# Kernel optimization log

Measured on AMD Instinct MI355X. Metric: run time of the kernel, lower is better.

Reference implementation:

```python
import jax, jax.numpy as jnp
import numpy as np

IN_CH = 64
INTER = IN_CH // 2
B, H, W = 2, 80, 80


def setup_inputs() -> dict:
    key = jax.random.key(0)
    k = jax.random.split(key, 5)
    s = 1.0 / np.sqrt(IN_CH)
    return {
        "x": jax.random.normal(k[0], (B, IN_CH, H, W), dtype=jnp.float32),
        "g_w": jax.random.normal(k[1], (INTER, IN_CH), dtype=jnp.float32) * s,
        "theta_w": jax.random.normal(k[2], (INTER, IN_CH), dtype=jnp.float32) * s,
        "phi_w": jax.random.normal(k[3], (INTER, IN_CH), dtype=jnp.float32) * s,
        "w_w": jax.random.normal(k[4], (IN_CH, INTER), dtype=jnp.float32) * (1.0 / np.sqrt(INTER)),
    }


def reference(x, g_w, theta_w, phi_w, w_w):
    # Non-local block: 1x1 convs (bias=False) are channel matmuls over N=H*W positions.
    Bc, C, Hh, Ww = x.shape
    N = Hh * Ww
    xf = x.reshape(Bc, C, N)                            # [B, C, N]
    g = jnp.einsum('ic,bcn->bni', g_w, xf)              # [B, N, inter]
    theta = jnp.einsum('ic,bcn->bni', theta_w, xf)      # [B, N, inter]
    phi = jnp.einsum('ic,bcn->bin', phi_w, xf)          # [B, inter, N]
    affinity = jax.nn.softmax(jnp.einsum('bni,bim->bnm', theta, phi), axis=-1)  # [B, N, N]
    y = jnp.einsum('bnm,bmi->bni', affinity, g)         # [B, N, inter]
    y = jnp.einsum('ci,bni->bcn', w_w, y).reshape(Bc, C, Hh, Ww)
    return x + y
```

## Files before the change

### kernel.cpp

```cpp
#include <hip/hip_runtime.h>
#include <math.h>

#define BATCH 2
#define CH    64
#define INTER 32
#define NPOS  6400
#define LOG2E 1.44269504088896f
#define SPLIT 10
#define TPB   5

typedef _Float16 f16x8 __attribute__((ext_vector_type(8)));
typedef _Float16 f16x2 __attribute__((ext_vector_type(2)));
typedef _Float16 h4    __attribute__((ext_vector_type(4)));
typedef float    f32x4 __attribute__((ext_vector_type(4)));

static __device__ __forceinline__ f16x2 pkrtz(float a, float b) {
    return __builtin_bit_cast(f16x2, __builtin_amdgcn_cvt_pkrtz(a, b));
}

__global__ __launch_bounds__(256) void nlb_proj_kernel(
    const float* __restrict__ x,
    const float* __restrict__ g_w,
    const float* __restrict__ th_w,
    const float* __restrict__ ph_w,
    _Float16* __restrict__ Qh, _Float16* __restrict__ Kh,
    _Float16* __restrict__ Vt)
{
    const int b  = blockIdx.z;
    const int p  = blockIdx.y;
    const int n0 = blockIdx.x * 64;
    const int t  = threadIdx.x;
    const int w  = __builtin_amdgcn_readfirstlane(t) >> 6;
    const int lane = t & 63;

    const float* wsrc = (p == 0) ? th_w : (p == 1) ? ph_w : g_w;
    const float* xg = x + (size_t)b * CH * NPOS + n0 + lane;

    float xr[64];
    #pragma unroll
    for (int c = 0; c < 64; c++) xr[c] = xg[(size_t)c * NPOS];

    __shared__ float buf[32][65];

    float accs[8];
    #pragma unroll
    for (int rr = 0; rr < 8; rr++) {
        const int row = w * 8 + rr;
        const float* wr = wsrc + row * 64;
        float a0 = 0.f, a1 = 0.f, a2 = 0.f, a3 = 0.f;
        #pragma unroll
        for (int c = 0; c < 16; c++) {
            a0 += wr[c]      * xr[c];
            a1 += wr[c + 16] * xr[c + 16];
            a2 += wr[c + 32] * xr[c + 32];
            a3 += wr[c + 48] * xr[c + 48];
        }
        accs[rr] = (a0 + a1) + (a2 + a3);
    }

    if (p == 2) {
        const int n   = n0 + lane;
        const int kk  = n & 127;
        const int g   = kk >> 4, qd = (kk >> 2) & 3, rr2 = kk & 3;
        const int slot = (g >> 1) * 32 + qd * 8 + (g & 1) * 4 + rr2;
        const size_t col = (size_t)(n >> 7) * 128 + slot;
        #pragma unroll
        for (int rr = 0; rr < 8; rr++)
            Vt[((size_t)b * 32 + w * 8 + rr) * NPOS + col] = (_Float16)accs[rr];
        return;
    }

    #pragma unroll
    for (int rr = 0; rr < 8; rr++) buf[w * 8 + rr][lane] = accs[rr];
    __syncthreads();

    const float scale = (p == 0) ? LOG2E : 1.f;
    _Float16* dst = (p == 0) ? Qh : Kh;
    const int pos = t >> 2, ic = t & 3;
    f16x8 hv;
    #pragma unroll
    for (int j = 0; j < 8; j++)
        hv[j] = (_Float16)(buf[ic * 8 + j][pos] * scale);
    *(f16x8*)(dst + ((size_t)b * NPOS + n0 + pos) * 32 + ic * 8) = hv;
}

__global__ __launch_bounds__(256) void nlb_flash_kernel(
    const _Float16* __restrict__ Qh, const _Float16* __restrict__ Kh,
    const _Float16* __restrict__ Vt,
    _Float16* __restrict__ Opart, float2* __restrict__ ml)
{
    __shared__ __align__(16) _Float16 ks[2][128][40];
    __shared__ __align__(16) _Float16 vs[2][32][136];

    const int b     = blockIdx.z;
    const int split = blockIdx.y;
    const int t     = threadIdx.x;
    const int w     = t >> 6;
    const int lane  = t & 63;
    const int n16   = lane & 15;
    const int quad  = lane >> 4;
    const int q0    = blockIdx.x * 64 + w * 16;

    const f16x8 qa = *(const f16x8*)(Qh + ((size_t)b * NPOS + q0 + n16) * 32 + quad * 8);

    const _Float16* KB = Kh + (size_t)b * NPOS * 32;
    const _Float16* VB = Vt + (size_t)b * 32 * NPOS;

    f32x4 o0 = (f32x4)0.f;
    f32x4 o1 = (f32x4)0.f;
    float runm = -1e30f, lsum = 0.f;

    const int key0 = t >> 2, part = t & 3, key1 = key0 + 64;
    const int dim0 = t >> 4, kp   = t & 15, dim1 = dim0 + 16;

    const int kt0 = split * TPB;
    f16x8 kr0, kr1, vr0, vr1;
    {
        const int k0 = kt0 * 128;
        kr0 = *(const f16x8*)(KB + (size_t)(k0 + key0) * 32 + part * 8);
        kr1 = *(const f16x8*)(KB + (size_t)(k0 + key1) * 32 + part * 8);
        vr0 = *(const f16x8*)(VB + (size_t)dim0 * NPOS + k0 + kp * 8);
        vr1 = *(const f16x8*)(VB + (size_t)dim1 * NPOS + k0 + kp * 8);
    }

    for (int i = 0; i < TPB; i++) {
        const int cur = i & 1;
        *(f16x8*)&ks[cur][key0][part * 8] = kr0;
        *(f16x8*)&ks[cur][key1][part * 8] = kr1;
        *(f16x8*)&vs[cur][dim0][kp * 8]   = vr0;
        *(f16x8*)&vs[cur][dim1][kp * 8]   = vr1;
        __syncthreads();

        if (i + 1 < TPB) {
            const int k0n = (kt0 + i + 1) * 128;
            kr0 = *(const f16x8*)(KB + (size_t)(k0n + key0) * 32 + part * 8);
            kr1 = *(const f16x8*)(KB + (size_t)(k0n + key1) * 32 + part * 8);
            vr0 = *(const f16x8*)(VB + (size_t)dim0 * NPOS + k0n + kp * 8);
            vr1 = *(const f16x8*)(VB + (size_t)dim1 * NPOS + k0n + kp * 8);
        }

        f32x4 sc[8];
        #pragma unroll
        for (int g = 0; g < 8; g++) {
            f16x8 kf = *(const f16x8*)&ks[cur][g * 16 + n16][quad * 8];
            f32x4 z = (f32x4)0.f;
            sc[g] = __builtin_amdgcn_mfma_f32_16x16x32_f16(kf, qa, z, 0, 0, 0);
        }

        float m = fmaxf(fmaxf(sc[0][0], sc[0][1]), fmaxf(sc[0][2], sc[0][3]));
        #pragma unroll
        for (int g = 1; g < 8; g++) {
            float mg = fmaxf(fmaxf(sc[g][0], sc[g][1]), fmaxf(sc[g][2], sc[g][3]));
            m = fmaxf(m, mg);
        }
        m = fmaxf(m, __shfl_xor(m, 16));
        m = fmaxf(m, __shfl_xor(m, 32));
        float nm = fmaxf(runm, m);
        float a  = __builtin_amdgcn_exp2f(runm - nm);
        runm = nm;
        float ls = 0.f;
        #pragma unroll
        for (int g = 0; g < 8; g++) {
            #pragma unroll
            for (int r = 0; r < 4; r++) {
                float p = __builtin_amdgcn_exp2f(sc[g][r] - nm);
                sc[g][r] = p;
                ls += p;
            }
        }
        lsum = lsum * a + ls;
        o0 *= a;
        o1 *= a;

        #pragma unroll
        for (int kc = 0; kc < 4; kc++) {
            union { f16x8 v; f16x2 h2[4]; } pb;
            pb.h2[0] = pkrtz(sc[kc * 2][0],     sc[kc * 2][1]);
            pb.h2[1] = pkrtz(sc[kc * 2][2],     sc[kc * 2][3]);
            pb.h2[2] = pkrtz(sc[kc * 2 + 1][0], sc[kc * 2 + 1][1]);
            pb.h2[3] = pkrtz(sc[kc * 2 + 1][2], sc[kc * 2 + 1][3]);
            f16x8 v0 = *(const f16x8*)&vs[cur][n16][kc * 32 + quad * 8];
            f16x8 v1 = *(const f16x8*)&vs[cur][16 + n16][kc * 32 + quad * 8];
            o0 = __builtin_amdgcn_mfma_f32_16x16x32_f16(v0, pb.v, o0, 0, 0, 0);
            o1 = __builtin_amdgcn_mfma_f32_16x16x32_f16(v1, pb.v, o1, 0, 0, 0);
        }
    }

    lsum += __shfl_xor(lsum, 16);
    lsum += __shfl_xor(lsum, 32);
    float invl = 1.f / lsum;
    const size_t base = ((size_t)(b * SPLIT + split) * NPOS + q0 + n16) * 32;
    h4 h0, h1;
    #pragma unroll
    for (int r = 0; r < 4; r++) {
        h0[r] = (_Float16)(o0[r] * invl);
        h1[r] = (_Float16)(o1[r] * invl);
    }
    *(h4*)(Opart + base + quad * 4)      = h0;
    *(h4*)(Opart + base + 16 + quad * 4) = h1;
    if (quad == 0)
        ml[(size_t)(b * SPLIT + split) * NPOS + q0 + n16] = make_float2(runm, lsum);
}

__global__ __launch_bounds__(256) void nlb_combine_kernel(
    const _Float16* __restrict__ Opart, const float2* __restrict__ ml,
    const float* __restrict__ w_w, const float* __restrict__ x,
    float* __restrict__ out)
{
    __shared__ float wf[64][33];
    __shared__ float wts[32][12];
    __shared__ float of[32][33];

    const int b  = blockIdx.y;
    const int q0 = blockIdx.x * 32;
    const int t  = threadIdx.x;

    for (int idx = t; idx < 2048; idx += 256) wf[idx >> 5][idx & 31] = w_w[idx];

    if (t < 32) {
        float2 v[SPLIT];
        float m = -1e30f;
        #pragma unroll
        for (int s = 0; s < SPLIT; s++) {
            v[s] = ml[(size_t)(b * SPLIT + s) * NPOS + q0 + t];
            m = fmaxf(m, v[s].x);
        }
        float suml = 0.f;
        #pragma unroll
        for (int s = 0; s < SPLIT; s++) {
            float wgt = __builtin_amdgcn_exp2f(v[s].x - m) * v[s].y;
            wts[t][s] = wgt;
            suml += wgt;
        }
        float inv = 1.f / suml;
        #pragma unroll
        for (int s = 0; s < SPLIT; s++) wts[t][s] *= inv;
    }
    __syncthreads();

    {
        const int q = t >> 3, dg = t & 7;
        float a0 = 0.f, a1 = 0.f, a2 = 0.f, a3 = 0.f;
        #pragma unroll
        for (int s = 0; s < SPLIT; s++) {
            h4 hv = *(const h4*)(Opart +
                ((size_t)(b * SPLIT + s) * NPOS + q0 + q) * 32 + dg * 4);
            float c = wts[q][s];
            a0 += c * (float)hv[0]; a1 += c * (float)hv[1];
            a2 += c * (float)hv[2]; a3 += c * (float)hv[3];
        }
        of[q][dg * 4]     = a0; of[q][dg * 4 + 1] = a1;
        of[q][dg * 4 + 2] = a2; of[q][dg * 4 + 3] = a3;
    }
    __syncthreads();

    {
        const int q = t & 31, cg = t >> 5;
        const float* xb = x   + (size_t)b * CH * NPOS + q0 + q;
        float*       ob = out + (size_t)b * CH * NPOS + q0 + q;
        #pragma unroll
        for (int cc = 0; cc < 8; cc++) {
            int ch = cg * 8 + cc;
            float acc = 0.f;
            #pragma unroll
            for (int i = 0; i < 32; i++) acc += wf[ch][i] * of[q][i];
            ob[(size_t)ch * NPOS] = acc + xb[(size_t)ch * NPOS];
        }
    }
}

extern "C" void kernel_launch(void* const* d_in, const int* in_sizes, int n_in,
                              void* d_out, int out_size, void* d_ws, size_t ws_size,
                              hipStream_t stream) {
    const float* x    = (const float*)d_in[0];
    const float* g_w  = (const float*)d_in[1];
    const float* th_w = (const float*)d_in[2];
    const float* ph_w = (const float*)d_in[3];
    const float* w_w  = (const float*)d_in[4];
    float* out = (float*)d_out;

    const size_t SZ = (size_t)BATCH * NPOS * INTER;
    _Float16* Qh = (_Float16*)d_ws;
    _Float16* Kh = Qh + SZ;
    _Float16* Vt = Kh + SZ;
    _Float16* Opart = Vt + SZ;
    float2*   ml    = (float2*)(Opart + SZ * SPLIT);

    nlb_proj_kernel<<<dim3(NPOS / 64, 3, BATCH), 256, 0, stream>>>(
        x, g_w, th_w, ph_w, Qh, Kh, Vt);
    nlb_flash_kernel<<<dim3(NPOS / 64, SPLIT, BATCH), 256, 0, stream>>>(
        Qh, Kh, Vt, Opart, ml);
    nlb_combine_kernel<<<dim3(NPOS / 32, BATCH), 256, 0, stream>>>(
        Opart, ml, w_w, x, out);
}
```

Measured before the change: 107.5 us.

## Fuse split-combine and output projection into flash kernel via last-block atomic counter

Removes the separate combine kernel. Each flash block bumps a per-query-block atomic counter after a threadfence, and the last of the SPLIT blocks to finish merges the partial outputs, applies the w_w projection and adds the residual. The counters are zeroed in the projection kernel. This saves one kernel launch and its gap, at the cost of an extra fence, atomics, a serialized tail on one block per query tile, and a union shared-memory layout.

```diff
diff --git a/kernel.cpp b/kernel.cpp
--- a/kernel.cpp
+++ b/kernel.cpp
@@ -8,6 +8,7 @@
 #define LOG2E 1.44269504088896f
 #define SPLIT 10
 #define TPB   5
+#define NQB   (NPOS / 64)
 
 typedef _Float16 f16x8 __attribute__((ext_vector_type(8)));
 typedef _Float16 f16x2 __attribute__((ext_vector_type(2)));
@@ -24,7 +25,7 @@
     const float* __restrict__ th_w,
     const float* __restrict__ ph_w,
     _Float16* __restrict__ Qh, _Float16* __restrict__ Kh,
-    _Float16* __restrict__ Vt)
+    _Float16* __restrict__ Vt, int* __restrict__ cnt)
 {
     const int b  = blockIdx.z;
     const int p  = blockIdx.y;
@@ -33,6 +34,8 @@
     const int w  = __builtin_amdgcn_readfirstlane(t) >> 6;
     const int lane = t & 63;
 
+    if (p == 0 && t == 0) cnt[b * NQB + blockIdx.x] = 0;
+
     const float* wsrc = (p == 0) ? th_w : (p == 1) ? ph_w : g_w;
     const float* xg = x + (size_t)b * CH * NPOS + n0 + lane;
 
@@ -84,13 +87,29 @@
     *(f16x8*)(dst + ((size_t)b * NPOS + n0 + pos) * 32 + ic * 8) = hv;
 }
 
+struct SmemFlash {
+    _Float16 ks[2][128][40];
+    _Float16 vs[2][32][136];
+};
+struct SmemTail {
+    float wf[64][33];
+    float wts[64][12];
+    float of[64][33];
+};
+
 __global__ __launch_bounds__(256) void nlb_flash_kernel(
     const _Float16* __restrict__ Qh, const _Float16* __restrict__ Kh,
     const _Float16* __restrict__ Vt,
-    _Float16* __restrict__ Opart, float2* __restrict__ ml)
+    _Float16* __restrict__ Opart, float2* __restrict__ ml,
+    int* __restrict__ cnt,
+    const float* __restrict__ w_w, const float* __restrict__ x,
+    float* __restrict__ out)
 {
-    __shared__ __align__(16) _Float16 ks[2][128][40];
-    __shared__ __align__(16) _Float16 vs[2][32][136];
+    constexpr size_t SMEM_BYTES =
+        sizeof(SmemFlash) > sizeof(SmemTail) ? sizeof(SmemFlash) : sizeof(SmemTail);
+    __shared__ __align__(16) char smem[SMEM_BYTES];
+    __shared__ int lastFlag;
+    SmemFlash* sf = (SmemFlash*)smem;
 
     const int b     = blockIdx.z;
     const int split = blockIdx.y;
@@ -125,10 +144,10 @@
 
     for (int i = 0; i < TPB; i++) {
         const int cur = i & 1;
-        *(f16x8*)&ks[cur][key0][part * 8] = kr0;
-        *(f16x8*)&ks[cur][key1][part * 8] = kr1;
-        *(f16x8*)&vs[cur][dim0][kp * 8]   = vr0;
-        *(f16x8*)&vs[cur][dim1][kp * 8]   = vr1;
+        *(f16x8*)&sf->ks[cur][key0][part * 8] = kr0;
+        *(f16x8*)&sf->ks[cur][key1][part * 8] = kr1;
+        *(f16x8*)&sf->vs[cur][dim0][kp * 8]   = vr0;
+        *(f16x8*)&sf->vs[cur][dim1][kp * 8]   = vr1;
         __syncthreads();
 
         if (i + 1 < TPB) {
@@ -142,7 +161,7 @@
         f32x4 sc[8];
         #pragma unroll
         for (int g = 0; g < 8; g++) {
-            f16x8 kf = *(const f16x8*)&ks[cur][g * 16 + n16][quad * 8];
+            f16x8 kf = *(const f16x8*)&sf->ks[cur][g * 16 + n16][quad * 8];
             f32x4 z = (f32x4)0.f;
             sc[g] = __builtin_amdgcn_mfma_f32_16x16x32_f16(kf, qa, z, 0, 0, 0);
         }
@@ -179,8 +198,8 @@
             pb.h2[1] = pkrtz(sc[kc * 2][2],     sc[kc * 2][3]);
             pb.h2[2] = pkrtz(sc[kc * 2 + 1][0], sc[kc * 2 + 1][1]);
             pb.h2[3] = pkrtz(sc[kc * 2 + 1][2], sc[kc * 2 + 1][3]);
-            f16x8 v0 = *(const f16x8*)&vs[cur][n16][kc * 32 + quad * 8];
-            f16x8 v1 = *(const f16x8*)&vs[cur][16 + n16][kc * 32 + quad * 8];
+            f16x8 v0 = *(const f16x8*)&sf->vs[cur][n16][kc * 32 + quad * 8];
+            f16x8 v1 = *(const f16x8*)&sf->vs[cur][16 + n16][kc * 32 + quad * 8];
             o0 = __builtin_amdgcn_mfma_f32_16x16x32_f16(v0, pb.v, o0, 0, 0, 0);
             o1 = __builtin_amdgcn_mfma_f32_16x16x32_f16(v1, pb.v, o1, 0, 0, 0);
         }
@@ -200,70 +219,72 @@
     *(h4*)(Opart + base + 16 + quad * 4) = h1;
     if (quad == 0)
         ml[(size_t)(b * SPLIT + split) * NPOS + q0 + n16] = make_float2(runm, lsum);
-}
-
-__global__ __launch_bounds__(256) void nlb_combine_kernel(
-    const _Float16* __restrict__ Opart, const float2* __restrict__ ml,
-    const float* __restrict__ w_w, const float* __restrict__ x,
-    float* __restrict__ out)
-{
-    __shared__ float wf[64][33];
-    __shared__ float wts[32][12];
-    __shared__ float of[32][33];
-
-    const int b  = blockIdx.y;
-    const int q0 = blockIdx.x * 32;
-    const int t  = threadIdx.x;
-
-    for (int idx = t; idx < 2048; idx += 256) wf[idx >> 5][idx & 31] = w_w[idx];
-
-    if (t < 32) {
+
+    __threadfence();
+    __syncthreads();
+    if (t == 0) {
+        int old = atomicAdd(&cnt[b * NQB + blockIdx.x], 1);
+        lastFlag = (old == SPLIT - 1);
+    }
+    __syncthreads();
+    if (!lastFlag) return;
+    __threadfence();
+
+    SmemTail* st = (SmemTail*)smem;
+    const int q0b = blockIdx.x * 64;
+
+    for (int idx = t; idx < 2048; idx += 256)
+        st->wf[idx >> 5][idx & 31] = w_w[idx];
+
+    if (t < 64) {
         float2 v[SPLIT];
         float m = -1e30f;
         #pragma unroll
         for (int s = 0; s < SPLIT; s++) {
-            v[s] = ml[(size_t)(b * SPLIT + s) * NPOS + q0 + t];
+            v[s] = ml[(size_t)(b * SPLIT + s) * NPOS + q0b + t];
             m = fmaxf(m, v[s].x);
         }
         float suml = 0.f;
         #pragma unroll
         for (int s = 0; s < SPLIT; s++) {
             float wgt = __builtin_amdgcn_exp2f(v[s].x - m) * v[s].y;
-            wts[t][s] = wgt;
+            st->wts[t][s] = wgt;
             suml += wgt;
         }
         float inv = 1.f / suml;
         #pragma unroll
-        for (int s = 0; s < SPLIT; s++) wts[t][s] *= inv;
+        for (int s = 0; s < SPLIT; s++) st->wts[t][s] *= inv;
     }
     __syncthreads();
 
     {
-        const int q = t >> 3, dg = t & 7;
-        float a0 = 0.f, a1 = 0.f, a2 = 0.f, a3 = 0.f;
+        const int q = t >> 2, dg = t & 3;
+        float acc[8];
+        #pragma unroll
+        for (int d = 0; d < 8; d++) acc[d] = 0.f;
         #pragma unroll
         for (int s = 0; s < SPLIT; s++) {
-            h4 hv = *(const h4*)(Opart +
-                ((size_t)(b * SPLIT + s) * NPOS + q0 + q) * 32 + dg * 4);
-            float c = wts[q][s];
-            a0 += c * (float)hv[0]; a1 += c * (float)hv[1];
-            a2 += c * (float)hv[2]; a3 += c * (float)hv[3];
-        }
-        of[q][dg * 4]     = a0; of[q][dg * 4 + 1] = a1;
-        of[q][dg * 4 + 2] = a2; of[q][dg * 4 + 3] = a3;
+            f16x8 hv = *(const f16x8*)(Opart +
+                ((size_t)(b * SPLIT + s) * NPOS + q0b + q) * 32 + dg * 8);
+            float c = st->wts[q][s];
+            #pragma unroll
+            for (int d = 0; d < 8; d++) acc[d] += c * (float)hv[d];
+        }
+        #pragma unroll
+        for (int d = 0; d < 8; d++) st->of[q][dg * 8 + d] = acc[d];
     }
     __syncthreads();
 
     {
-        const int q = t & 31, cg = t >> 5;
-        const float* xb = x   + (size_t)b * CH * NPOS + q0 + q;
-        float*       ob = out + (size_t)b * CH * NPOS + q0 + q;
-        #pragma unroll
-        for (int cc = 0; cc < 8; cc++) {
-            int ch = cg * 8 + cc;
+        const int q = t & 63, cg = t >> 6;
+        const float* xb = x   + (size_t)b * CH * NPOS + q0b + q;
+        float*       ob = out + (size_t)b * CH * NPOS + q0b + q;
+        #pragma unroll
+        for (int cc = 0; cc < 16; cc++) {
+            int ch = cg * 16 + cc;
             float acc = 0.f;
             #pragma unroll
-            for (int i = 0; i < 32; i++) acc += wf[ch][i] * of[q][i];
+            for (int i = 0; i < 32; i++) acc += st->wf[ch][i] * st->of[q][i];
             ob[(size_t)ch * NPOS] = acc + xb[(size_t)ch * NPOS];
         }
     }
@@ -285,11 +306,10 @@
     _Float16* Vt = Kh + SZ;
     _Float16* Opart = Vt + SZ;
     float2*   ml    = (float2*)(Opart + SZ * SPLIT);
+    int*      cnt   = (int*)(ml + (size_t)BATCH * SPLIT * NPOS);
 
     nlb_proj_kernel<<<dim3(NPOS / 64, 3, BATCH), 256, 0, stream>>>(
-        x, g_w, th_w, ph_w, Qh, Kh, Vt);
-    nlb_flash_kernel<<<dim3(NPOS / 64, SPLIT, BATCH), 256, 0, stream>>>(
-        Qh, Kh, Vt, Opart, ml);
-    nlb_combine_kernel<<<dim3(NPOS / 32, BATCH), 256, 0, stream>>>(
-        Opart, ml, w_w, x, out);
+        x, g_w, th_w, ph_w, Qh, Kh, Vt, cnt);
+    nlb_flash_kernel<<<dim3(NQB, SPLIT, BATCH), 256, 0, stream>>>(
+        Qh, Kh, Vt, Opart, ml, cnt, w_w, x, out);
 }
```

Result: slower. 322.6 us (+200.0%).
